# Performance work log

Measured on AMD Instinct MI355X. Metric: run time of the kernel, lower is better.

Reference implementation:

```python
import jax, jax.numpy as jnp
import numpy as np

NUM_HEADS = 16
NEG_INF = -1e18


def setup_inputs() -> dict:
    key = jax.random.key(0)
    ks = jax.random.split(key, 9)
    T, B, D = 2048, 2, 1024
    s = 1.0 / np.sqrt(D)
    return {
        "query": jax.random.normal(ks[0], (T, B, D), jnp.float32),
        "q_w": jax.random.normal(ks[1], (D, D), jnp.float32) * s,
        "q_b": jax.random.normal(ks[2], (D,), jnp.float32) * 0.02,
        "k_w": jax.random.normal(ks[3], (D, D), jnp.float32) * s,
        "k_b": jax.random.normal(ks[4], (D,), jnp.float32) * 0.02,
        "v_w": jax.random.normal(ks[5], (D, D), jnp.float32) * s,
        "v_b": jax.random.normal(ks[6], (D,), jnp.float32) * 0.02,
        "out_w": jax.random.normal(ks[7], (D, D), jnp.float32) * s,
        "out_b": jax.random.normal(ks[8], (D,), jnp.float32) * 0.02,
    }


def reference(query, q_w, q_b, k_w, k_b, v_w, v_b, out_w, out_b):
    # query: [T, B, D] (Time x Batch x Channel). Self-attention, causal mask,
    # dropout=0, need_weights=True.
    T, B, D = query.shape
    H = NUM_HEADS
    hd = D // H
    scaling = 1.0 / jnp.sqrt(jnp.asarray(hd, query.dtype))

    q = (query @ q_w.T + q_b) * scaling
    k = query @ k_w.T + k_b
    v = query @ v_w.T + v_b

    def split_heads(x):  # [T, B, D] -> [B, H, T, hd]
        return x.reshape(T, B, H, hd).transpose(1, 2, 0, 3)

    qh, kh, vh = split_heads(q), split_heads(k), split_heads(v)

    # scores: [B, H, T, T]
    scores = jnp.einsum("bhtd,bhsd->bhts", qh, kh)
    causal = jnp.triu(jnp.full((T, T), NEG_INF, dtype=scores.dtype), k=1)
    scores = scores + causal

    probs = jax.nn.softmax(scores, axis=-1)
    attn = jnp.einsum("bhts,bhsd->bhtd", probs, vh)  # [B, H, T, hd]
    attn = attn.transpose(2, 0, 1, 3).reshape(T, B, D)
    out = attn @ out_w.T + out_b

    # averaged attention weights over heads: [B, T, T]
    avg_weights = probs.sum(axis=1) / H
    return out, avg_weights
```

## Files before the change

### kernel.cpp

```cpp
#include <hip/hip_runtime.h>
#include <hip/hip_bf16.h>
#include <stdint.h>

typedef __hip_bfloat16 bf16;
using short8 = __attribute__((ext_vector_type(8))) short;
using f32x4  = __attribute__((ext_vector_type(4))) float;

#define TDIM 2048
#define BDIM 2
#define DDIM 1024
#define HNUM 16
#define HD   64
#define MDIM 4096
#define M0   16.0f
#define L2E  1.44269504088896f
#define M0B  23.0831207f

__device__ __forceinline__ f32x4 mfma16(short8 a, short8 b, f32x4 c) {
  return __builtin_amdgcn_mfma_f32_16x16x32_bf16(a, b, c, 0, 0, 0);
}

__device__ __forceinline__ float fexp2(float s) {
  return __builtin_amdgcn_exp2f(__builtin_fmaf(s, L2E, -M0B));
}

#define GLD16(G, L)                                              \
  __builtin_amdgcn_global_load_lds(                              \
      (const __attribute__((address_space(1))) void*)(G),        \
      (__attribute__((address_space(3))) void*)(L), 16, 0, 0)

union S8 { short8 v; bf16 h[8]; };
union P4 { uint2 u; bf16 h[4]; };

__global__ __launch_bounds__(256) void cast_all_kernel(
    const float* __restrict__ q, const float* __restrict__ wq,
    const float* __restrict__ wk, const float* __restrict__ wv,
    const float* __restrict__ wo, bf16* __restrict__ dst) {
  int t4 = blockIdx.x * blockDim.x + threadIdx.x;
  int idx = t4 * 4;
  const float* s;
  if (idx < 4194304)      s = q  + idx;
  else if (idx < 5242880) s = wq + (idx - 4194304);
  else if (idx < 6291456) s = wk + (idx - 5242880);
  else if (idx < 7340032) s = wv + (idx - 6291456);
  else                    s = wo + (idx - 7340032);
  float4 v = *(const float4*)s;
  union { ushort4 u; bf16 b[4]; } pk;
  pk.b[0] = __float2bfloat16(v.x);
  pk.b[1] = __float2bfloat16(v.y);
  pk.b[2] = __float2bfloat16(v.z);
  pk.b[3] = __float2bfloat16(v.w);
  *(ushort4*)(dst + idx) = pk.u;
}

__global__ __launch_bounds__(256, 2) void qkv_kernel(
    const bf16* __restrict__ X, const bf16* __restrict__ Wq,
    const bf16* __restrict__ Wk, const bf16* __restrict__ Wv,
    const float* __restrict__ qb, const float* __restrict__ kb,
    const float* __restrict__ vb, bf16* __restrict__ Qo,
    bf16* __restrict__ Ko, bf16* __restrict__ Vto) {
  __shared__ __align__(16) bf16 Xs[128][72];
  __shared__ __align__(16) bf16 Qs[64][72];
  __shared__ __align__(16) bf16 Ks[64][72];
  __shared__ __align__(16) bf16 Vs[64][72];
  const int tid  = threadIdx.x;
  const int lane = tid & 63, wave = tid >> 6;
  const int m0 = blockIdx.y * 128, n0 = blockIdx.x * 64;
  const int wm = (wave >> 1) * 64, wn = (wave & 1) * 32;
  const int fr = lane & 15, quad = lane >> 4, q8 = quad * 8;
  const int r = tid >> 3, cc = (tid & 7) * 8;
  f32x4 aq[4][2] = {}, ak[4][2] = {}, av[2][4] = {};
  const bf16* xp = X  + (size_t)(m0 + r) * DDIM + cc;
  const bf16* qp = Wq + (size_t)(n0 + r) * DDIM + cc;
  const bf16* kp = Wk + (size_t)(n0 + r) * DDIM + cc;
  const bf16* vp = Wv + (size_t)(n0 + r) * DDIM + cc;
  uint4 xv0, xv1, xv2, xv3, qv0, qv1, kv0, kv1, vv0, vv1;
#define QKV_LD(K0)                                                  \
  do {                                                              \
    xv0 = *(const uint4*)(xp + (K0));                               \
    xv1 = *(const uint4*)(xp + (size_t)32 * DDIM + (K0));           \
    xv2 = *(const uint4*)(xp + (size_t)64 * DDIM + (K0));           \
    xv3 = *(const uint4*)(xp + (size_t)96 * DDIM + (K0));           \
    qv0 = *(const uint4*)(qp + (K0));                               \
    qv1 = *(const uint4*)(qp + (size_t)32 * DDIM + (K0));           \
    kv0 = *(const uint4*)(kp + (K0));                               \
    kv1 = *(const uint4*)(kp + (size_t)32 * DDIM + (K0));           \
    vv0 = *(const uint4*)(vp + (K0));                               \
    vv1 = *(const uint4*)(vp + (size_t)32 * DDIM + (K0));           \
  } while (0)
  QKV_LD(0);
  for (int k0 = 0; k0 < DDIM; k0 += 64) {
    __syncthreads();
    *(uint4*)&Xs[r][cc]      = xv0;
    *(uint4*)&Xs[r + 32][cc] = xv1;
    *(uint4*)&Xs[r + 64][cc] = xv2;
    *(uint4*)&Xs[r + 96][cc] = xv3;
    *(uint4*)&Qs[r][cc]      = qv0;
    *(uint4*)&Qs[r + 32][cc] = qv1;
    *(uint4*)&Ks[r][cc]      = kv0;
    *(uint4*)&Ks[r + 32][cc] = kv1;
    *(uint4*)&Vs[r][cc]      = vv0;
    *(uint4*)&Vs[r + 32][cc] = vv1;
    __syncthreads();
    if (k0 + 64 < DDIM) QKV_LD(k0 + 64);
#pragma unroll
    for (int kk = 0; kk < 2; kk++) {
      const int ko = kk * 32 + q8;
      short8 xf[4], qf[2], kf[2], vf[2];
#pragma unroll
      for (int i = 0; i < 4; i++)
        xf[i] = *(const short8*)&Xs[wm + i * 16 + fr][ko];
#pragma unroll
      for (int j = 0; j < 2; j++) {
        qf[j] = *(const short8*)&Qs[wn + j * 16 + fr][ko];
        kf[j] = *(const short8*)&Ks[wn + j * 16 + fr][ko];
        vf[j] = *(const short8*)&Vs[wn + j * 16 + fr][ko];
      }
#pragma unroll
      for (int i = 0; i < 4; i++)
#pragma unroll
        for (int j = 0; j < 2; j++) {
          aq[i][j] = mfma16(xf[i], qf[j], aq[i][j]);
          ak[i][j] = mfma16(xf[i], kf[j], ak[i][j]);
          av[j][i] = mfma16(vf[j], xf[i], av[j][i]);
        }
    }
  }
#undef QKV_LD
#pragma unroll
  for (int mt = 0; mt < 4; mt++)
#pragma unroll
    for (int nt = 0; nt < 2; nt++)
#pragma unroll
      for (int i = 0; i < 4; i++) {
        int gm = m0 + wm + mt * 16 + quad * 4 + i;
        int gn = n0 + wn + nt * 16 + fr;
        int t = gm >> 1, bb = gm & 1, h = gn >> 6, e = gn & 63;
        size_t o = ((size_t)(bb * HNUM + h) * TDIM + t) * HD + e;
        Qo[o] = __float2bfloat16((aq[mt][nt][i] + qb[gn]) * 0.125f);
        Ko[o] = __float2bfloat16(ak[mt][nt][i] + kb[gn]);
      }
#pragma unroll
  for (int vt = 0; vt < 2; vt++)
#pragma unroll
    for (int xt = 0; xt < 4; xt++)
#pragma unroll
      for (int i = 0; i < 4; i++) {
        int gf = n0 + wn + vt * 16 + quad * 4 + i;
        int gt = m0 + wm + xt * 16 + fr;
        int t = gt >> 1, bb = gt & 1, h = gf >> 6, e = gf & 63;
        Vto[((size_t)(bb * HNUM + h) * HD + e) * TDIM + t] =
            __float2bfloat16(av[vt][xt][i] + vb[gf]);
      }
}

__global__ __launch_bounds__(256) void combine_kernel(
    const bf16* __restrict__ P0, const bf16* __restrict__ P1,
    const float* __restrict__ l0buf, const float* __restrict__ l1buf,
    bf16* __restrict__ A) {
  const int idx = (blockIdx.x * 256 + threadIdx.x) * 8;
  const int m = idx >> 10, col = idx & 1023;
  const int t = m >> 1, bb = m & 1, h = col >> 6;
  const size_t li = (size_t)(bb * HNUM + h) * TDIM + t;
  const float inv = 1.0f / (l0buf[li] + l1buf[li]);
  S8 a0, a1, w;
  a0.v = *(const short8*)&P0[idx];
  a1.v = *(const short8*)&P1[idx];
#pragma unroll
  for (int k = 0; k < 8; k++)
    w.h[k] = __float2bfloat16(
        (__bfloat162float(a0.h[k]) + __bfloat162float(a1.h[k])) * inv);
  *(short8*)&A[idx] = w.v;
}

__global__ __launch_bounds__(256) void gemm_out_kernel(
    const bf16* __restrict__ A, const bf16* __restrict__ Bw,
    const float* __restrict__ bias, float* __restrict__ of32) {
  __shared__ __align__(16) bf16 As[64][72];
  __shared__ __align__(16) bf16 Bs[64][72];
  const int tid  = threadIdx.x;
  const int lane = tid & 63, wave = tid >> 6;
  const int m0 = blockIdx.y * 64, n0 = blockIdx.x * 64;
  const int wm = (wave >> 1) * 32, wn = (wave & 1) * 32;
  const int fr = lane & 15, quad = lane >> 4, q8 = quad * 8;
  const int ldr = tid >> 3, ldc = (tid & 7) * 8;
  f32x4 acc[2][2] = {};
  const bf16* ap0 = A + (size_t)(m0 + ldr) * DDIM + ldc;
  const bf16* ap1 = ap0 + (size_t)32 * DDIM;
  const bf16* bp0 = Bw + (size_t)(n0 + ldr) * DDIM + ldc;
  const bf16* bp1 = bp0 + (size_t)32 * DDIM;
  uint4 av0, av1, bv0, bv1;
#define OUT_LD(K0)                                  \
  do {                                              \
    av0 = *(const uint4*)(ap0 + (K0));              \
    av1 = *(const uint4*)(ap1 + (K0));              \
    bv0 = *(const uint4*)(bp0 + (K0));              \
    bv1 = *(const uint4*)(bp1 + (K0));              \
  } while (0)
  OUT_LD(0);
  for (int k0 = 0; k0 < DDIM; k0 += 64) {
    __syncthreads();
    *(uint4*)&As[ldr][ldc]      = av0;
    *(uint4*)&As[ldr + 32][ldc] = av1;
    *(uint4*)&Bs[ldr][ldc]      = bv0;
    *(uint4*)&Bs[ldr + 32][ldc] = bv1;
    __syncthreads();
    if (k0 + 64 < DDIM) OUT_LD(k0 + 64);
#pragma unroll
    for (int kk = 0; kk < 2; kk++) {
      const int ko = kk * 32 + q8;
      short8 af0, af1, bf0, bf1;
      af0 = *(const short8*)&As[wm + fr][ko];
      af1 = *(const short8*)&As[wm + 16 + fr][ko];
      bf0 = *(const short8*)&Bs[wn + fr][ko];
      bf1 = *(const short8*)&Bs[wn + 16 + fr][ko];
      acc[0][0] = mfma16(af0, bf0, acc[0][0]);
      acc[0][1] = mfma16(af0, bf1, acc[0][1]);
      acc[1][0] = mfma16(af1, bf0, acc[1][0]);
      acc[1][1] = mfma16(af1, bf1, acc[1][1]);
    }
  }
#undef OUT_LD
#pragma unroll
  for (int mt = 0; mt < 2; mt++)
#pragma unroll
    for (int nt = 0; nt < 2; nt++)
#pragma unroll
      for (int i = 0; i < 4; i++) {
        int gm = m0 + wm + mt * 16 + quad * 4 + i;
        int gn = n0 + wn + nt * 16 + fr;
        of32[(size_t)gm * DDIM + gn] = acc[mt][nt][i] + bias[gn];
      }
}

__global__ __launch_bounds__(256) void attn_split_kernel(
    const bf16* __restrict__ Q, const bf16* __restrict__ K,
    const bf16* __restrict__ Vt, bf16* __restrict__ P0o,
    bf16* __restrict__ P1o, float* __restrict__ l0buf,
    float* __restrict__ l1buf) {
  __shared__ __align__(16) bf16 Ks[2][64][40];
  __shared__ __align__(16) bf16 Vs[2][64][40];
  __shared__ __align__(16) bf16 pt[4][32][72];
  const int tid = threadIdx.x, lane = tid & 63, wave = tid >> 6;
  const int bid = blockIdx.x;
  const int part = bid & 1, bh = (bid >> 1) & 31, t128 = 15 - (bid >> 6);
  const int b = bh >> 4, h = bh & 15;
  const int t0 = t128 * 128 + wave * 32;
  const int fr = lane & 15, quad = lane >> 4, q8 = quad * 8;
  const bf16* Qp = Q + ((size_t)bh * TDIM + t0) * HD;
  const bf16* Kp = K + (size_t)bh * TDIM * HD;
  const bf16* Vp = Vt + (size_t)bh * HD * TDIM;
  short8 aq[2][2];
  aq[0][0] = *(const short8*)&Qp[fr * HD + q8];
  aq[0][1] = *(const short8*)&Qp[fr * HD + 32 + q8];
  aq[1][0] = *(const short8*)&Qp[(16 + fr) * HD + q8];
  aq[1][1] = *(const short8*)&Qp[(16 + fr) * HD + 32 + q8];
  const int Cb = 2 * t128 + 2, C0 = t128 + 1;
  const int clo = part ? C0 : 0, chi = part ? Cb : C0;
  const int sr0 = tid >> 3, scc = (tid & 7) * 8, sr1 = sr0 + 32;
  const int ssub = scc >> 5, scol = scc & 31;
  f32x4 oacc[2][4] = {};
  float lsum[2] = {0.f, 0.f};
  uint4 kv0, kv1, vv0, vv1;
  auto ldglob = [&](int c) {
    int s0 = c * 64;
    kv0 = *(const uint4*)&Kp[(size_t)(s0 + sr0) * HD + scc];
    kv1 = *(const uint4*)&Kp[(size_t)(s0 + sr1) * HD + scc];
    vv0 = *(const uint4*)&Vp[(size_t)sr0 * TDIM + s0 + scc];
    vv1 = *(const uint4*)&Vp[(size_t)sr1 * TDIM + s0 + scc];
  };
  ldglob(clo);
  for (int c = clo; c < chi; c++) {
    __syncthreads();
    *(uint4*)&Ks[ssub][sr0][scol] = kv0;
    *(uint4*)&Ks[ssub][sr1][scol] = kv1;
    *(uint4*)&Vs[ssub][sr0][scol] = vv0;
    *(uint4*)&Vs[ssub][sr1][scol] = vv1;
    __syncthreads();
    if (c + 1 < chi) ldglob(c + 1);
    const int s0 = c * 64;
    if (s0 > t0 + 31) continue;
    f32x4 scT[2][4] = {};
#pragma unroll
    for (int j = 0; j < 4; j++) {
      short8 k0f = *(const short8*)&Ks[0][j * 16 + fr][q8];
      short8 k1f = *(const short8*)&Ks[1][j * 16 + fr][q8];
      scT[0][j] = mfma16(k0f, aq[0][0], scT[0][j]);
      scT[0][j] = mfma16(k1f, aq[0][1], scT[0][j]);
      scT[1][j] = mfma16(k0f, aq[1][0], scT[1][j]);
      scT[1][j] = mfma16(k1f, aq[1][1], scT[1][j]);
    }
#pragma unroll
    for (int g = 0; g < 2; g++) {
      const int tg = t0 + g * 16;
#pragma unroll
      for (int j = 0; j < 4; j++) {
        const int sj = s0 + j * 16;
        P4 pk;
        if (sj > tg + 15) {
          pk.u = make_uint2(0u, 0u);
        } else if (sj + 15 <= tg) {
#pragma unroll
          for (int i = 0; i < 4; i++) {
            float p = fexp2(scT[g][j][i]);
            lsum[g] += p;
            pk.h[i] = __float2bfloat16(p);
          }
        } else {
          const int t_row = tg + fr;
          const int s_base = sj + quad * 4;
#pragma unroll
          for (int i = 0; i < 4; i++) {
            float p = 0.f;
            if (s_base + i <= t_row) {
              p = fexp2(scT[g][j][i]);
              lsum[g] += p;
            }
            pk.h[i] = __float2bfloat16(p);
          }
        }
        *(uint2*)&pt[wave][g * 16 + fr][j * 16 + quad * 4] = pk.u;
      }
    }
#pragma unroll
    for (int c2 = 0; c2 < 2; c2++) {
      short8 ap0 = *(const short8*)&pt[wave][fr][c2 * 32 + q8];
      short8 ap1 = *(const short8*)&pt[wave][16 + fr][c2 * 32 + q8];
#pragma unroll
      for (int nt = 0; nt < 4; nt++) {
        short8 vf = *(const short8*)&Vs[c2][nt * 16 + fr][q8];
        oacc[0][nt] = mfma16(ap0, vf, oacc[0][nt]);
        oacc[1][nt] = mfma16(ap1, vf, oacc[1][nt]);
      }
    }
  }
  float lr[2];
#pragma unroll
  for (int g = 0; g < 2; g++) {
    float l = lsum[g];
    l += __shfl_xor(l, 16);
    l += __shfl_xor(l, 32);
    lr[g] = l;
  }
  bf16*  Op = part ? P1o : P0o;
  float* lb = part ? l1buf : l0buf;
#pragma unroll
  for (int g = 0; g < 2; g++)
#pragma unroll
    for (int nt = 0; nt < 4; nt++)
#pragma unroll
      for (int i = 0; i < 4; i++) {
        int t_row = t0 + g * 16 + quad * 4 + i;
        int col = h * HD + nt * 16 + fr;
        Op[((size_t)t_row * BDIM + b) * DDIM + col] =
            __float2bfloat16(oacc[g][nt][i]);
      }
  if (quad == 0) {
    lb[(size_t)bh * TDIM + t0 + fr]      = lr[0];
    lb[(size_t)bh * TDIM + t0 + 16 + fr] = lr[1];
  }
}

__global__ __launch_bounds__(128) void avg_kernel(
    const bf16* __restrict__ Q, const bf16* __restrict__ K,
    const float* __restrict__ l0buf, const float* __restrict__ l1buf,
    float* __restrict__ avgw) {
  const int tid = threadIdx.x;
  int gid = blockIdx.x;
  if (gid >= 1056) {
    int z = gid - 1056;
    const int b = (z >= 496) ? 1 : 0;
    if (b) z -= 496;
    int ti = 0;
    while (ti < 30 && (31 * (ti + 1) - (ti + 1) * ti / 2) <= z) ti++;
    int si = ti + 1 + (z - (31 * ti - ti * (ti - 1) / 2));
    int t0b = ti * 64, s0 = si * 64;
    float* avp = avgw + (size_t)b * TDIM * TDIM;
#pragma unroll
    for (int k = 0; k < 8; k++) {
      int e = (tid + k * 128) * 4;
      *(float4*)&avp[(size_t)(t0b + (e >> 6)) * TDIM + s0 + (e & 63)] =
          make_float4(0.f, 0.f, 0.f, 0.f);
    }
    return;
  }
  const int b = (gid >= 528) ? 1 : 0;
  int r = gid - (b ? 528 : 0);
  int ti = 0;
  while (ti < 31 && (ti + 1) * (ti + 2) / 2 <= r) ti++;
  const int si = r - ti * (ti + 1) / 2;
  const int t0b = ti * 64, s0 = si * 64;
  float* avp = avgw + (size_t)b * TDIM * TDIM;

  __shared__ __align__(16) bf16 Ks[2][64][64];
  __shared__ float sinvl[HNUM][64];
#pragma unroll
  for (int k = 0; k < 8; k++) {
    int idx = tid + k * 128;
    size_t li = (size_t)(b * HNUM + (idx >> 6)) * TDIM + t0b + (idx & 63);
    sinvl[idx >> 6][idx & 63] = 1.0f / (l0buf[li] + l1buf[li]);
  }
  const int lane = tid & 63, wave = tid >> 6;
  const int fr = lane & 15, quad = lane >> 4, q8 = quad * 8;
  const int tw = t0b + wave * 32;
  const int srow8 = lane >> 3;
  const int scol = ((lane & 7) ^ (srow8 & 7)) * 8;
  const int sl0 = ((quad)     ^ (fr & 7)) * 8;
  const int sl1 = ((4 + quad) ^ (fr & 7)) * 8;
  const bf16* Qb = Q + (size_t)b * HNUM * TDIM * HD;
  const bf16* Kb = K + (size_t)b * HNUM * TDIM * HD;
#define AVG_STAGEK(B, HH)                                               \
  do {                                                                  \
    const bf16* Kh_ = Kb + (size_t)(HH) * TDIM * HD;                    \
    GLD16(Kh_ + (size_t)(s0 + 32 * wave + srow8) * HD + scol,           \
          &Ks[B][32 * wave][0]);                                        \
    GLD16(Kh_ + (size_t)(s0 + 32 * wave + 8 + srow8) * HD + scol,       \
          &Ks[B][32 * wave + 8][0]);                                    \
    GLD16(Kh_ + (size_t)(s0 + 32 * wave + 16 + srow8) * HD + scol,      \
          &Ks[B][32 * wave + 16][0]);                                   \
    GLD16(Kh_ + (size_t)(s0 + 32 * wave + 24 + srow8) * HD + scol,      \
          &Ks[B][32 * wave + 24][0]);                                   \
  } while (0)
#define AVG_LOADQ(P, HH)                                                   \
  do {                                                                    \
    const bf16* Qh_ = Qb + (size_t)(HH) * TDIM * HD;                      \
    P[0][0] = *(const short8*)&Qh_[(size_t)(tw + fr) * HD + q8];          \
    P[0][1] = *(const short8*)&Qh_[(size_t)(tw + fr) * HD + 32 + q8];     \
    P[1][0] = *(const short8*)&Qh_[(size_t)(tw + 16 + fr) * HD + q8];     \
    P[1][1] = *(const short8*)&Qh_[(size_t)(tw + 16 + fr) * HD + 32 + q8];\
  } while (0)
  bool dead[2][4], full[2][4];
#pragma unroll
  for (int ts = 0; ts < 2; ts++)
#pragma unroll
    for (int cg = 0; cg < 4; cg++) {
      dead[ts][cg] = (s0 + cg * 16 > tw + ts * 16 + 15);
      full[ts][cg] = (s0 + cg * 16 + 15 <= tw + ts * 16);
    }
  short8 qf[2][2][2];
  AVG_STAGEK(0, 0);
  AVG_LOADQ(qf[0], 0);
  f32x4 facc[2][4] = {};
#pragma unroll
  for (int hh = 0; hh < HNUM; hh++) {
    const int cur = hh & 1;
    __syncthreads();
    if (hh + 1 < HNUM) {
      AVG_STAGEK(cur ^ 1, hh + 1);
      AVG_LOADQ(qf[cur ^ 1], hh + 1);
    }
    short8 kb0[4], kb1[4];
#pragma unroll
    for (int cg = 0; cg < 4; cg++) {
      kb0[cg] = *(const short8*)&Ks[cur][cg * 16 + fr][sl0];
      kb1[cg] = *(const short8*)&Ks[cur][cg * 16 + fr][sl1];
    }
#pragma unroll
    for (int ts = 0; ts < 2; ts++) {
      f32x4 sv = *(const f32x4*)&sinvl[hh][32 * wave + ts * 16 + quad * 4];
#pragma unroll
      for (int cg = 0; cg < 4; cg++) {
        if (dead[ts][cg]) continue;
        f32x4 sc = {};
        sc = mfma16(qf[cur][ts][0], kb0[cg], sc);
        sc = mfma16(qf[cur][ts][1], kb1[cg], sc);
        if (full[ts][cg]) {
#pragma unroll
          for (int i = 0; i < 4; i++)
            facc[ts][cg][i] += fexp2(sc[i]) * sv[i];
        } else {
#pragma unroll
          for (int i = 0; i < 4; i++)
            if (s0 + cg * 16 + fr <= tw + ts * 16 + quad * 4 + i)
              facc[ts][cg][i] += fexp2(sc[i]) * sv[i];
        }
      }
    }
  }
#undef AVG_STAGEK
#undef AVG_LOADQ
#pragma unroll
  for (int ts = 0; ts < 2; ts++)
#pragma unroll
    for (int cg = 0; cg < 4; cg++)
#pragma unroll
      for (int i = 0; i < 4; i++)
        avp[(size_t)(tw + ts * 16 + quad * 4 + i) * TDIM + s0 + cg * 16 + fr] =
            facc[ts][cg][i] * 0.0625f;
}

extern "C" void kernel_launch(void* const* d_in, const int* in_sizes, int n_in,
                              void* d_out, int out_size, void* d_ws, size_t ws_size,
                              hipStream_t stream) {
  const float* q   = (const float*)d_in[0];
  const float* q_w = (const float*)d_in[1];
  const float* q_b = (const float*)d_in[2];
  const float* k_w = (const float*)d_in[3];
  const float* k_b = (const float*)d_in[4];
  const float* v_w = (const float*)d_in[5];
  const float* v_b = (const float*)d_in[6];
  const float* o_w = (const float*)d_in[7];
  const float* o_b = (const float*)d_in[8];
  float* out = (float*)d_out;
  float* avg = out + (size_t)MDIM * DDIM;

  bf16* ws  = (bf16*)d_ws;
  bf16* Xbf = ws;
  bf16* Wq  = ws + 4194304;
  bf16* Wk  = ws + 5242880;
  bf16* Wv  = ws + 6291456;
  bf16* Wo  = ws + 7340032;
  bf16* Qw  = ws + 8388608;
  bf16* Kw  = ws + 12582912;
  bf16* Vt  = ws + 16777216;
  bf16* P1  = ws + 20971520;
  bf16* P0  = ws;
  bf16* Ab  = ws + 16777216;
  float* l0 = (float*)(ws + 4194304);
  float* l1 = (float*)(ws + 4325376);

  cast_all_kernel<<<8192, 256, 0, stream>>>(q, q_w, k_w, v_w, o_w, Xbf);
  qkv_kernel<<<dim3(16, 32), 256, 0, stream>>>(Xbf, Wq, Wk, Wv, q_b, k_b, v_b,
                                               Qw, Kw, Vt);
  attn_split_kernel<<<1024, 256, 0, stream>>>(Qw, Kw, Vt, P0, P1, l0, l1);
  combine_kernel<<<2048, 256, 0, stream>>>(P0, P1, l0, l1, Ab);
  avg_kernel<<<2048, 128, 0, stream>>>(Qw, Kw, l0, l1, avg);
  gemm_out_kernel<<<dim3(16, 64), 256, 0, stream>>>(Ab, Wo, o_b, out);
}
```

Measured before the change: 224.3 us.

## Merge output GEMM and averaged-weights kernels into one interleaved launch

Replaces the separate avg_kernel and gemm_out_kernel launches with a single tail_kernel of 2048 blocks. Odd blocks run one output-projection GEMM tile, and even blocks run two 128-thread avg-weight tiles packed into one 256-thread block using shared memory carved from a common buffer. The aim is to overlap the memory-bound averaged-weights work with the MFMA-bound GEMM and remove one launch and its tail. In exchange, every block reserves the larger shared allocation, and the `__syncthreads` inside the packed avg halves now synchronizes both halves together.

```diff
diff --git a/kernel.cpp b/kernel.cpp
--- a/kernel.cpp
+++ b/kernel.cpp
@@ -173,66 +173,6 @@
   *(short8*)&A[idx] = w.v;
 }
 
-__global__ __launch_bounds__(256) void gemm_out_kernel(
-    const bf16* __restrict__ A, const bf16* __restrict__ Bw,
-    const float* __restrict__ bias, float* __restrict__ of32) {
-  __shared__ __align__(16) bf16 As[64][72];
-  __shared__ __align__(16) bf16 Bs[64][72];
-  const int tid  = threadIdx.x;
-  const int lane = tid & 63, wave = tid >> 6;
-  const int m0 = blockIdx.y * 64, n0 = blockIdx.x * 64;
-  const int wm = (wave >> 1) * 32, wn = (wave & 1) * 32;
-  const int fr = lane & 15, quad = lane >> 4, q8 = quad * 8;
-  const int ldr = tid >> 3, ldc = (tid & 7) * 8;
-  f32x4 acc[2][2] = {};
-  const bf16* ap0 = A + (size_t)(m0 + ldr) * DDIM + ldc;
-  const bf16* ap1 = ap0 + (size_t)32 * DDIM;
-  const bf16* bp0 = Bw + (size_t)(n0 + ldr) * DDIM + ldc;
-  const bf16* bp1 = bp0 + (size_t)32 * DDIM;
-  uint4 av0, av1, bv0, bv1;
-#define OUT_LD(K0)                                  \
-  do {                                              \
-    av0 = *(const uint4*)(ap0 + (K0));              \
-    av1 = *(const uint4*)(ap1 + (K0));              \
-    bv0 = *(const uint4*)(bp0 + (K0));              \
-    bv1 = *(const uint4*)(bp1 + (K0));              \
-  } while (0)
-  OUT_LD(0);
-  for (int k0 = 0; k0 < DDIM; k0 += 64) {
-    __syncthreads();
-    *(uint4*)&As[ldr][ldc]      = av0;
-    *(uint4*)&As[ldr + 32][ldc] = av1;
-    *(uint4*)&Bs[ldr][ldc]      = bv0;
-    *(uint4*)&Bs[ldr + 32][ldc] = bv1;
-    __syncthreads();
-    if (k0 + 64 < DDIM) OUT_LD(k0 + 64);
-#pragma unroll
-    for (int kk = 0; kk < 2; kk++) {
-      const int ko = kk * 32 + q8;
-      short8 af0, af1, bf0, bf1;
-      af0 = *(const short8*)&As[wm + fr][ko];
-      af1 = *(const short8*)&As[wm + 16 + fr][ko];
-      bf0 = *(const short8*)&Bs[wn + fr][ko];
-      bf1 = *(const short8*)&Bs[wn + 16 + fr][ko];
-      acc[0][0] = mfma16(af0, bf0, acc[0][0]);
-      acc[0][1] = mfma16(af0, bf1, acc[0][1]);
-      acc[1][0] = mfma16(af1, bf0, acc[1][0]);
-      acc[1][1] = mfma16(af1, bf1, acc[1][1]);
-    }
-  }
-#undef OUT_LD
-#pragma unroll
-  for (int mt = 0; mt < 2; mt++)
-#pragma unroll
-    for (int nt = 0; nt < 2; nt++)
-#pragma unroll
-      for (int i = 0; i < 4; i++) {
-        int gm = m0 + wm + mt * 16 + quad * 4 + i;
-        int gn = n0 + wn + nt * 16 + fr;
-        of32[(size_t)gm * DDIM + gn] = acc[mt][nt][i] + bias[gn];
-      }
-}
-
 __global__ __launch_bounds__(256) void attn_split_kernel(
     const bf16* __restrict__ Q, const bf16* __restrict__ K,
     const bf16* __restrict__ Vt, bf16* __restrict__ P0o,
@@ -361,16 +301,82 @@
   }
 }
 
-__global__ __launch_bounds__(128) void avg_kernel(
-    const bf16* __restrict__ Q, const bf16* __restrict__ K,
+__global__ __launch_bounds__(256) void tail_kernel(
+    const bf16* __restrict__ A, const bf16* __restrict__ Bw,
+    const float* __restrict__ bias, float* __restrict__ of32,
+    const bf16* __restrict__ Q, const bf16* __restrict__ Kw,
     const float* __restrict__ l0buf, const float* __restrict__ l1buf,
     float* __restrict__ avgw) {
+  __shared__ __align__(16) char smem[40960];
   const int tid = threadIdx.x;
-  int gid = blockIdx.x;
-  if (gid >= 1056) {
-    int z = gid - 1056;
-    const int b = (z >= 496) ? 1 : 0;
-    if (b) z -= 496;
+  const int gid = blockIdx.x;
+
+  if (gid & 1) {
+    const int g = gid >> 1;
+    bf16 (*As)[72] = (bf16(*)[72])smem;
+    bf16 (*Bs)[72] = (bf16(*)[72])(smem + 9216);
+    const int lane = tid & 63, wave = tid >> 6;
+    const int m0 = (g >> 4) * 64, n0 = (g & 15) * 64;
+    const int wm = (wave >> 1) * 32, wn = (wave & 1) * 32;
+    const int fr = lane & 15, quad = lane >> 4, q8 = quad * 8;
+    const int ldr = tid >> 3, ldc = (tid & 7) * 8;
+    f32x4 acc[2][2] = {};
+    const bf16* ap0 = A + (size_t)(m0 + ldr) * DDIM + ldc;
+    const bf16* ap1 = ap0 + (size_t)32 * DDIM;
+    const bf16* bp0 = Bw + (size_t)(n0 + ldr) * DDIM + ldc;
+    const bf16* bp1 = bp0 + (size_t)32 * DDIM;
+    uint4 av0, av1, bv0, bv1;
+#define OUT_LD(K0)                                  \
+    do {                                            \
+      av0 = *(const uint4*)(ap0 + (K0));            \
+      av1 = *(const uint4*)(ap1 + (K0));            \
+      bv0 = *(const uint4*)(bp0 + (K0));            \
+      bv1 = *(const uint4*)(bp1 + (K0));            \
+    } while (0)
+    OUT_LD(0);
+    for (int k0 = 0; k0 < DDIM; k0 += 64) {
+      __syncthreads();
+      *(uint4*)&As[ldr][ldc]      = av0;
+      *(uint4*)&As[ldr + 32][ldc] = av1;
+      *(uint4*)&Bs[ldr][ldc]      = bv0;
+      *(uint4*)&Bs[ldr + 32][ldc] = bv1;
+      __syncthreads();
+      if (k0 + 64 < DDIM) OUT_LD(k0 + 64);
+#pragma unroll
+      for (int kk = 0; kk < 2; kk++) {
+        const int ko = kk * 32 + q8;
+        short8 af0, af1, bf0, bf1;
+        af0 = *(const short8*)&As[wm + fr][ko];
+        af1 = *(const short8*)&As[wm + 16 + fr][ko];
+        bf0 = *(const short8*)&Bs[wn + fr][ko];
+        bf1 = *(const short8*)&Bs[wn + 16 + fr][ko];
+        acc[0][0] = mfma16(af0, bf0, acc[0][0]);
+        acc[0][1] = mfma16(af0, bf1, acc[0][1]);
+        acc[1][0] = mfma16(af1, bf0, acc[1][0]);
+        acc[1][1] = mfma16(af1, bf1, acc[1][1]);
+      }
+    }
+#undef OUT_LD
+#pragma unroll
+    for (int mt = 0; mt < 2; mt++)
+#pragma unroll
+      for (int nt = 0; nt < 2; nt++)
+#pragma unroll
+        for (int i = 0; i < 4; i++) {
+          int gm = m0 + wm + mt * 16 + quad * 4 + i;
+          int gn = n0 + wn + nt * 16 + fr;
+          of32[(size_t)gm * DDIM + gn] = acc[mt][nt][i] + bias[gn];
+        }
+    return;
+  }
+
+  const int p = gid >> 1;
+  const int pr = tid >> 7, t2 = tid & 127;
+  if (p >= 528) {
+    int zp = p - 528;
+    const int b = (zp >= 248) ? 1 : 0;
+    if (b) zp -= 248;
+    int z = 2 * zp + pr;
     int ti = 0;
     while (ti < 30 && (31 * (ti + 1) - (ti + 1) * ti / 2) <= z) ti++;
     int si = ti + 1 + (z - (31 * ti - ti * (ti - 1) / 2));
@@ -378,48 +384,48 @@
     float* avp = avgw + (size_t)b * TDIM * TDIM;
 #pragma unroll
     for (int k = 0; k < 8; k++) {
-      int e = (tid + k * 128) * 4;
+      int e = (t2 + k * 128) * 4;
       *(float4*)&avp[(size_t)(t0b + (e >> 6)) * TDIM + s0 + (e & 63)] =
           make_float4(0.f, 0.f, 0.f, 0.f);
     }
     return;
   }
-  const int b = (gid >= 528) ? 1 : 0;
-  int r = gid - (b ? 528 : 0);
+  const int b = (p >= 264) ? 1 : 0;
+  const int r = 2 * (p - 264 * b) + pr;
   int ti = 0;
   while (ti < 31 && (ti + 1) * (ti + 2) / 2 <= r) ti++;
   const int si = r - ti * (ti + 1) / 2;
   const int t0b = ti * 64, s0 = si * 64;
   float* avp = avgw + (size_t)b * TDIM * TDIM;
 
-  __shared__ __align__(16) bf16 Ks[2][64][64];
-  __shared__ float sinvl[HNUM][64];
+  bf16 (*Ksb)[64][64] = (bf16(*)[64][64])(smem + pr * 16384);
+  float (*sinv)[64]   = (float(*)[64])(smem + 32768 + pr * 4096);
 #pragma unroll
   for (int k = 0; k < 8; k++) {
-    int idx = tid + k * 128;
+    int idx = t2 + k * 128;
     size_t li = (size_t)(b * HNUM + (idx >> 6)) * TDIM + t0b + (idx & 63);
-    sinvl[idx >> 6][idx & 63] = 1.0f / (l0buf[li] + l1buf[li]);
-  }
-  const int lane = tid & 63, wave = tid >> 6;
+    sinv[idx >> 6][idx & 63] = 1.0f / (l0buf[li] + l1buf[li]);
+  }
+  const int lane = t2 & 63, wv = t2 >> 6;
   const int fr = lane & 15, quad = lane >> 4, q8 = quad * 8;
-  const int tw = t0b + wave * 32;
+  const int tw = t0b + wv * 32;
   const int srow8 = lane >> 3;
   const int scol = ((lane & 7) ^ (srow8 & 7)) * 8;
   const int sl0 = ((quad)     ^ (fr & 7)) * 8;
   const int sl1 = ((4 + quad) ^ (fr & 7)) * 8;
-  const bf16* Qb = Q + (size_t)b * HNUM * TDIM * HD;
-  const bf16* Kb = K + (size_t)b * HNUM * TDIM * HD;
+  const bf16* Qb = Q  + (size_t)b * HNUM * TDIM * HD;
+  const bf16* Kb = Kw + (size_t)b * HNUM * TDIM * HD;
 #define AVG_STAGEK(B, HH)                                               \
   do {                                                                  \
     const bf16* Kh_ = Kb + (size_t)(HH) * TDIM * HD;                    \
-    GLD16(Kh_ + (size_t)(s0 + 32 * wave + srow8) * HD + scol,           \
-          &Ks[B][32 * wave][0]);                                        \
-    GLD16(Kh_ + (size_t)(s0 + 32 * wave + 8 + srow8) * HD + scol,       \
-          &Ks[B][32 * wave + 8][0]);                                    \
-    GLD16(Kh_ + (size_t)(s0 + 32 * wave + 16 + srow8) * HD + scol,      \
-          &Ks[B][32 * wave + 16][0]);                                   \
-    GLD16(Kh_ + (size_t)(s0 + 32 * wave + 24 + srow8) * HD + scol,      \
-          &Ks[B][32 * wave + 24][0]);                                   \
+    GLD16(Kh_ + (size_t)(s0 + 32 * wv + srow8) * HD + scol,             \
+          &Ksb[B][32 * wv][0]);                                         \
+    GLD16(Kh_ + (size_t)(s0 + 32 * wv + 8 + srow8) * HD + scol,         \
+          &Ksb[B][32 * wv + 8][0]);                                     \
+    GLD16(Kh_ + (size_t)(s0 + 32 * wv + 16 + srow8) * HD + scol,        \
+          &Ksb[B][32 * wv + 16][0]);                                    \
+    GLD16(Kh_ + (size_t)(s0 + 32 * wv + 24 + srow8) * HD + scol,        \
+          &Ksb[B][32 * wv + 24][0]);                                    \
   } while (0)
 #define AVG_LOADQ(P, HH)                                                   \
   do {                                                                    \
@@ -452,12 +458,12 @@
     short8 kb0[4], kb1[4];
 #pragma unroll
     for (int cg = 0; cg < 4; cg++) {
-      kb0[cg] = *(const short8*)&Ks[cur][cg * 16 + fr][sl0];
-      kb1[cg] = *(const short8*)&Ks[cur][cg * 16 + fr][sl1];
+      kb0[cg] = *(const short8*)&Ksb[cur][cg * 16 + fr][sl0];
+      kb1[cg] = *(const short8*)&Ksb[cur][cg * 16 + fr][sl1];
     }
 #pragma unroll
     for (int ts = 0; ts < 2; ts++) {
-      f32x4 sv = *(const f32x4*)&sinvl[hh][32 * wave + ts * 16 + quad * 4];
+      f32x4 sv = *(const f32x4*)&sinv[hh][32 * wv + ts * 16 + quad * 4];
 #pragma unroll
       for (int cg = 0; cg < 4; cg++) {
         if (dead[ts][cg]) continue;
@@ -524,6 +530,5 @@
                                                Qw, Kw, Vt);
   attn_split_kernel<<<1024, 256, 0, stream>>>(Qw, Kw, Vt, P0, P1, l0, l1);
   combine_kernel<<<2048, 256, 0, stream>>>(P0, P1, l0, l1, Ab);
-  avg_kernel<<<2048, 128, 0, stream>>>(Qw, Kw, l0, l1, avg);
-  gemm_out_kernel<<<dim3(16, 64), 256, 0, stream>>>(Ab, Wo, o_b, out);
-}
+  tail_kernel<<<2048, 256, 0, stream>>>(Ab, Wo, o_b, out, Qw, Kw, l0, l1, avg);
+}
```

Measured after the change: 223.6 us. No clear change (-0.3%).
